# Kernel tuning notes

Hardware: AMD Instinct MI355X
Metric: run time of the kernel (lower is better)

## Reference

```python
import jax, jax.numpy as jnp
import numpy as np


def gcn_conv(x, edge_index, W, b):
    """PyG GCNConv: add self-loops, symmetric deg^{-1/2} normalization,
    linear transform, then scatter-add aggregation, plus bias."""
    n = x.shape[0]
    loops = jnp.arange(n, dtype=edge_index.dtype)
    src = jnp.concatenate([edge_index[0], loops])  # [E+N]
    dst = jnp.concatenate([edge_index[1], loops])
    ones = jnp.ones(src.shape[0], dtype=x.dtype)
    deg = jax.ops.segment_sum(ones, dst, num_segments=n)  # in-degree incl. self-loop
    dinv = jax.lax.rsqrt(jnp.maximum(deg, 1e-12))
    norm = dinv[src] * dinv[dst]  # [E+N]
    h = x @ W  # transform first (out_dim <= in_dim), [N, out]
    msg = h[src] * norm[:, None]  # gather + scale
    out = jax.ops.segment_sum(msg, dst, num_segments=n)  # scatter-add
    return out + b


def setup_inputs() -> dict:
    key = jax.random.key(0)
    ks = jax.random.split(key, 8)
    N, E, D_IN, D_OUT = 100000, 6400000, 32, 4
    x = jax.random.normal(ks[0], (N, D_IN), dtype=jnp.float32)
    edge_index = jax.random.randint(ks[1], (2, E), 0, N, dtype=jnp.int64)
    s1 = 1.0 / np.sqrt(D_IN)
    s2 = 1.0 / np.sqrt(16)
    s3 = 1.0 / np.sqrt(8)
    W1 = jax.random.uniform(ks[2], (D_IN, 16), jnp.float32, -s1, s1)
    b1 = jnp.zeros((16,), jnp.float32)
    W2 = jax.random.uniform(ks[3], (16, 8), jnp.float32, -s2, s2)
    b2 = jnp.zeros((8,), jnp.float32)
    Wfc = jax.random.uniform(ks[4], (8, D_OUT), jnp.float32, -s3, s3)
    bfc = jax.random.uniform(ks[5], (D_OUT,), jnp.float32, -s3, s3)
    return {"x": x, "edge_index": edge_index, "W1": W1, "b1": b1,
            "W2": W2, "b2": b2, "Wfc": Wfc, "bfc": bfc}


def reference(x, edge_index, W1, b1, W2, b2, Wfc, bfc):
    h = jax.nn.relu(gcn_conv(x, edge_index, W1, b1))
    h = jax.nn.relu(gcn_conv(h, edge_index, W2, b2))
    return h @ Wfc + bfc
```

## Files before the change

kernel.cpp:

```cpp
#include <hip/hip_runtime.h>
#include <hip/hip_fp16.h>

#define BLK 256
#define SHIFT 8
#define BSZ 256
#define MAXB 512
#define SRCBITS 17
#define SRCMASK ((1u << SRCBITS) - 1u)
#define TILE2 16384
#define BT 1024
#define LCAP 18432


__global__ __launch_bounds__(BT) void k_binA2(const int* __restrict__ src,
                                              const int* __restrict__ dst, int E, int N,
                                              unsigned* __restrict__ binned,
                                              int* __restrict__ bofs) {
    __shared__ int cnt[MAXB];
    __shared__ int sscan[MAXB];
    __shared__ int excl[MAXB];
    __shared__ unsigned sw[TILE2];
    int t = threadIdx.x;
    if (t < MAXB) cnt[t] = 0;
    __syncthreads();
    size_t tb = (size_t)blockIdx.x * TILE2;
    unsigned wv[16];
    int rkbk[16];
#pragma unroll
    for (int q = 0; q < 4; ++q) {
        int i4 = t + q * BT;
        size_t e0 = tb + (size_t)i4 * 4;
        int4 s4, d4;
        bool vec = (e0 + 4 <= (size_t)E);
        if (vec) {
            s4 = ((const int4*)src)[tb / 4 + i4];
            d4 = ((const int4*)dst)[tb / 4 + i4];
        }
#pragma unroll
        for (int j = 0; j < 4; ++j) {
            int idx = q * 4 + j;
            rkbk[idx] = -1;
            size_t e = e0 + j;
            int d = -1, s = -1;
            if (vec) {
                d = (j == 0) ? d4.x : (j == 1) ? d4.y : (j == 2) ? d4.z : d4.w;
                s = (j == 0) ? s4.x : (j == 1) ? s4.y : (j == 2) ? s4.z : s4.w;
            } else if (e < (size_t)E) {
                d = dst[e]; s = src[e];
            }
            if ((unsigned)d < (unsigned)N && (unsigned)s < (unsigned)N) {
                int b = d >> SHIFT;
                wv[idx] = (unsigned)s | ((unsigned)(d & (BSZ - 1)) << SRCBITS);
                int r = atomicAdd(&cnt[b], 1);
                rkbk[idx] = (r << 9) | b;
            }
        }
    }
    __syncthreads();
    if (t < MAXB) sscan[t] = cnt[t];
    __syncthreads();
    for (int off = 1; off < MAXB; off <<= 1) {
        int u = 0;
        if (t < MAXB && t >= off) u = sscan[t - off];
        __syncthreads();
        if (t < MAXB) sscan[t] += u;
        __syncthreads();
    }
    if (t < MAXB) excl[t] = sscan[t] - cnt[t];
    __syncthreads();
    int total = sscan[MAXB - 1];
#pragma unroll
    for (int idx = 0; idx < 16; ++idx) {
        int rb = rkbk[idx];
        if (rb >= 0) sw[excl[rb & 511] + (rb >> 9)] = wv[idx];
    }
    __syncthreads();
    int nq = total >> 2;
    for (int p = t; p < nq; p += BT) {
        uint4 v = *(const uint4*)&sw[p << 2];
        *(uint4*)(binned + tb + ((size_t)p << 2)) = v;
    }
    for (int p = (nq << 2) + t; p < total; p += BT) binned[tb + p] = sw[p];
    size_t bo = (size_t)blockIdx.x * (MAXB + 1);
    if (t < MAXB) bofs[bo + t] = excl[t];
    if (t == 0) bofs[bo + MAXB] = total;
}

__global__ __launch_bounds__(MAXB) void k_bsum(const int* __restrict__ bofs, int ntiles,
                                               int* __restrict__ btot) {
    int t = threadIdx.x;
    int c = 0;
    for (int tl = blockIdx.x; tl < ntiles; tl += gridDim.x) {
        size_t bo = (size_t)tl * (MAXB + 1);
        c += bofs[bo + t + 1] - bofs[bo + t];
    }
    if (c) atomicAdd(&btot[t], c);
}

__global__ __launch_bounds__(MAXB) void k_bscan(const int* __restrict__ btot,
                                                int* __restrict__ base) {
    __shared__ int s[MAXB];
    int t = threadIdx.x;
    int v = btot[t];
    s[t] = v;
    __syncthreads();
    for (int off = 1; off < MAXB; off <<= 1) {
        int u = (t >= off) ? s[t - off] : 0;
        __syncthreads();
        s[t] += u;
        __syncthreads();
    }
    base[t] = s[t] - v;
    if (t == MAXB - 1) base[MAXB] = s[t];
}


__global__ __launch_bounds__(1024) void k_buildB4(const unsigned* __restrict__ binned,
                                                  const int* __restrict__ bofs,
                                                  const int* __restrict__ baseB,
                                                  int ntiles, int N,
                                                  float* __restrict__ dinv,
                                                  int* __restrict__ rp,
                                                  unsigned* __restrict__ csr) {
    __shared__ int h[BSZ];
    __shared__ int sc[BSZ];
    __shared__ int cnt[BSZ];
    extern __shared__ unsigned lcsr[];
    int b = blockIdx.x;
    int t = threadIdx.x;
    int gb = b << SHIFT;
    if (t < BSZ) h[t] = 0;
    __syncthreads();
    int lane = t & 63, wid = t >> 6;
    int sub = lane >> 4, sl = lane & 15;
    for (int S = wid * 4 + sub; S < ntiles; S += 64) {
        size_t bo = (size_t)S * (MAXB + 1);
        int st = bofs[bo + b], en = bofs[bo + b + 1];
        size_t base = (size_t)S * TILE2;
        int k = st + sl;
        for (; k + 16 < en; k += 32) {
            unsigned v0 = binned[base + k];
            unsigned v1 = binned[base + k + 16];
            atomicAdd(&h[v0 >> SRCBITS], 1);
            atomicAdd(&h[v1 >> SRCBITS], 1);
        }
        if (k < en) atomicAdd(&h[binned[base + k] >> SRCBITS], 1);
    }
    __syncthreads();
    if (t < BSZ) sc[t] = h[t];
    __syncthreads();
    for (int off = 1; off < BSZ; off <<= 1) {
        int u = 0;
        if (t < BSZ && t >= off) u = sc[t - off];
        __syncthreads();
        if (t < BSZ) sc[t] += u;
        __syncthreads();
    }
    int bb = baseB[b];
    int total = sc[BSZ - 1];
    if (t < BSZ) {
        int v = h[t];
        int excl = sc[t] - v;
        int gnode = gb + t;
        if (gnode < N) {
            rp[gnode] = bb + excl;
            dinv[gnode] = rsqrtf((float)v + 1.0f);
        }
        if (t == BSZ - 1) {
            int endn = gb + BSZ;
            if (endn > N) endn = N;
            rp[endn] = bb + total;
        }
        cnt[t] = excl;
    }
    __syncthreads();
    bool big = (total > LCAP);
    for (int S = wid * 4 + sub; S < ntiles; S += 64) {
        size_t bo = (size_t)S * (MAXB + 1);
        int st = bofs[bo + b], en = bofs[bo + b + 1];
        size_t base = (size_t)S * TILE2;
        int k = st + sl;
        for (; k + 16 < en; k += 32) {
            unsigned v0 = binned[base + k];
            unsigned v1 = binned[base + k + 16];
            int p0 = atomicAdd(&cnt[v0 >> SRCBITS], 1);
            int p1 = atomicAdd(&cnt[v1 >> SRCBITS], 1);
            unsigned w0 = (v0 & SRCMASK) << 5;
            unsigned w1 = (v1 & SRCMASK) << 5;
            if (!big) { lcsr[p0] = w0; lcsr[p1] = w1; }
            else      { csr[bb + p0] = w0; csr[bb + p1] = w1; }
        }
        if (k < en) {
            unsigned v = binned[base + k];
            int pos = atomicAdd(&cnt[v >> SRCBITS], 1);
            unsigned w = (v & SRCMASK) << 5;
            if (!big) lcsr[pos] = w;
            else      csr[bb + pos] = w;
        }
    }
    __syncthreads();
    if (!big) {
        int h0 = ((bb + 3) & ~3) - bb;
        if (h0 > total) h0 = total;
        if (t < h0) csr[bb + t] = lcsr[t];
        int rem = total - h0;
        int nq = (rem > 0) ? (rem >> 2) : 0;
        for (int p = t; p < nq; p += 1024) {
            int lp = h0 + (p << 2);
            uint4 v = make_uint4(lcsr[lp], lcsr[lp + 1], lcsr[lp + 2], lcsr[lp + 3]);
            *(uint4*)(csr + bb + lp) = v;
        }
        for (int p = h0 + (nq << 2) + t; p < total; p += 1024) csr[bb + p] = lcsr[p];
    }
}


union Pk8 { __half h[8]; uint4 u; };
union H2U { unsigned u; __half2 h; };

__global__ __launch_bounds__(BLK) void k_transform1h(const float* __restrict__ x,
                                                     const float* __restrict__ W1,
                                                     const float* __restrict__ dinv,
                                                     __half* __restrict__ g1h, int N) {
    __shared__ float sW[32 * 16];
    for (int t = threadIdx.x; t < 512; t += BLK) sW[t] = W1[t];
    __syncthreads();
    int i = blockIdx.x * BLK + threadIdx.x;
    if (i >= N) return;
    float xr[32];
    const float4* xp = (const float4*)(x + (size_t)i * 32);
#pragma unroll
    for (int q = 0; q < 8; ++q) {
        float4 v = xp[q];
        xr[4*q] = v.x; xr[4*q+1] = v.y; xr[4*q+2] = v.z; xr[4*q+3] = v.w;
    }
    float di = dinv[i];
    Pk8 p0, p1;
#pragma unroll
    for (int j = 0; j < 16; ++j) {
        float a = 0.f;
#pragma unroll
        for (int k = 0; k < 32; ++k) a += xr[k] * sW[k * 16 + j];
        if (j < 8) p0.h[j] = __float2half_rn(a * di);
        else       p1.h[j - 8] = __float2half_rn(a * di);
    }
    uint4* gp = (uint4*)(g1h + (size_t)i * 16);
    gp[0] = p0.u;
    gp[1] = p1.u;
}


__global__ __launch_bounds__(BLK) void k_agg1(const int* __restrict__ rp,
                                              const unsigned* __restrict__ csr,
                                              const __half* __restrict__ g1h,
                                              const float* __restrict__ dinv,
                                              const float* __restrict__ b1,
                                              const float* __restrict__ W2,
                                              float* __restrict__ g2, int N) {
    __shared__ float sW[16 * 8];
    __shared__ float sb[16];
    if (threadIdx.x < 128) sW[threadIdx.x] = W2[threadIdx.x];
    if (threadIdx.x < 16) sb[threadIdx.x] = b1[threadIdx.x];
    __syncthreads();
    int wid = blockIdx.x * (BLK / 32) + (threadIdx.x >> 5);
    if (wid >= N) return;
    int alane = threadIdx.x & 63;
    int lane = threadIdx.x & 31;
    int c4 = lane & 3;
    int slot = lane >> 2;
    const char* gbase = (const char*)g1h;
    int foff = c4 << 3;
    int base_ = rp[wid], end = rp[wid + 1];
    float a0 = 0.f, a1 = 0.f, a2 = 0.f, a3 = 0.f;
    int k = base_ + slot;
    for (; k + 8 < end; k += 16) {
        unsigned v0 = csr[k], v1 = csr[k + 8];
        uint2 u0 = *(const uint2*)(gbase + v0 + foff);
        uint2 u1 = *(const uint2*)(gbase + v1 + foff);
        H2U x0, x1, y0, y1;
        x0.u = u0.x; y0.u = u0.y; x1.u = u1.x; y1.u = u1.y;
        float2 f0 = __half22float2(x0.h), f1 = __half22float2(y0.h);
        float2 f2 = __half22float2(x1.h), f3 = __half22float2(y1.h);
        a0 += f0.x + f2.x; a1 += f0.y + f2.y;
        a2 += f1.x + f3.x; a3 += f1.y + f3.y;
    }
    if (k < end) {
        unsigned v0 = csr[k];
        uint2 u0 = *(const uint2*)(gbase + v0 + foff);
        H2U x0, y0;
        x0.u = u0.x; y0.u = u0.y;
        float2 f0 = __half22float2(x0.h), f1 = __half22float2(y0.h);
        a0 += f0.x; a1 += f0.y; a2 += f1.x; a3 += f1.y;
    }
#pragma unroll
    for (int m = 4; m <= 16; m <<= 1) {
        a0 += __shfl_xor(a0, m);
        a1 += __shfl_xor(a1, m);
        a2 += __shfl_xor(a2, m);
        a3 += __shfl_xor(a3, m);
    }
    float di = dinv[wid];
    uint2 su = *(const uint2*)(gbase + ((size_t)wid << 5) + foff);
    H2U sx, sy;
    sx.u = su.x; sy.u = su.y;
    float2 sf0 = __half22float2(sx.h), sf1 = __half22float2(sy.h);
    float hh[4];
    hh[0] = fmaxf((a0 + sf0.x) * di + sb[4*c4+0], 0.f);
    hh[1] = fmaxf((a1 + sf0.y) * di + sb[4*c4+1], 0.f);
    hh[2] = fmaxf((a2 + sf1.x) * di + sb[4*c4+2], 0.f);
    hh[3] = fmaxf((a3 + sf1.y) * di + sb[4*c4+3], 0.f);
    int g4 = alane & ~3;
    int o = lane & 7;
    float a = 0.f;
#pragma unroll
    for (int kk = 0; kk < 16; ++kk) {
        float hv = __shfl(hh[kk & 3], g4 + (kk >> 2));
        a += hv * sW[kk * 8 + o];
    }
    if (lane < 8) g2[(size_t)wid * 8 + lane] = a * di;
}

__global__ __launch_bounds__(BLK) void k_agg2(const int* __restrict__ rp,
                                              const unsigned* __restrict__ csr,
                                              const float* __restrict__ g2,
                                              const float* __restrict__ dinv,
                                              const float* __restrict__ b2,
                                              const float* __restrict__ Wfc,
                                              const float* __restrict__ bfc,
                                              float* __restrict__ out, int N) {
    __shared__ float sW[8 * 4];
    __shared__ float sb2[8];
    __shared__ float sbf[4];
    if (threadIdx.x < 32) sW[threadIdx.x] = Wfc[threadIdx.x];
    if (threadIdx.x < 8) sb2[threadIdx.x] = b2[threadIdx.x];
    if (threadIdx.x < 4) sbf[threadIdx.x] = bfc[threadIdx.x];
    __syncthreads();
    int wid = blockIdx.x * (BLK / 32) + (threadIdx.x >> 5);
    if (wid >= N) return;
    int alane = threadIdx.x & 63;
    int lane = threadIdx.x & 31;
    int c4 = lane & 3;
    int slot = lane >> 2;
    const char* gbase = (const char*)g2;
    int foff = c4 << 3;
    int base_ = rp[wid], end = rp[wid + 1];
    float a0 = 0.f, a1 = 0.f;
    int k = base_ + slot;
    for (; k + 8 < end; k += 16) {
        unsigned v0 = csr[k], v1 = csr[k + 8];
        float2 f0 = *(const float2*)(gbase + v0 + foff);
        float2 f1 = *(const float2*)(gbase + v1 + foff);
        a0 += f0.x + f1.x;
        a1 += f0.y + f1.y;
    }
    if (k < end) {
        unsigned v0 = csr[k];
        float2 f0 = *(const float2*)(gbase + v0 + foff);
        a0 += f0.x; a1 += f0.y;
    }
#pragma unroll
    for (int m = 4; m <= 16; m <<= 1) {
        a0 += __shfl_xor(a0, m);
        a1 += __shfl_xor(a1, m);
    }
    float di = dinv[wid];
    float2 sf = *(const float2*)(gbase + ((size_t)wid << 5) + foff);
    float hh[2];
    hh[0] = fmaxf((a0 + sf.x) * di + sb2[2*c4+0], 0.f);
    hh[1] = fmaxf((a1 + sf.y) * di + sb2[2*c4+1], 0.f);
    int g4 = alane & ~3;
    int o = lane & 3;
    float a = 0.f;
#pragma unroll
    for (int j = 0; j < 8; ++j) {
        float hv = __shfl(hh[j & 1], g4 + (j >> 1));
        a += hv * sW[j * 4 + o];
    }
    if (lane < 4) out[(size_t)wid * 4 + lane] = a + sbf[lane];
}


__global__ __launch_bounds__(BLK) void k_count(const int* __restrict__ dst, int E, int N,
                                               float* __restrict__ cnt) {
    int i = blockIdx.x * BLK + threadIdx.x;
    if (i < E) {
        int d = dst[i];
        if ((unsigned)d < (unsigned)N) atomicAdd(&cnt[d], 1.0f);
    }
}
__global__ __launch_bounds__(BLK) void k_dinv_f(float* __restrict__ cnt, int N) {
    int i = blockIdx.x * BLK + threadIdx.x;
    if (i < N) cnt[i] = rsqrtf(cnt[i] + 1.0f);
}
__global__ __launch_bounds__(BLK) void k_transform1(const float* __restrict__ x,
                                                    const float* __restrict__ W1,
                                                    const float* __restrict__ dinv,
                                                    float* __restrict__ g1, int N) {
    __shared__ float sW[32 * 16];
    for (int t = threadIdx.x; t < 512; t += BLK) sW[t] = W1[t];
    __syncthreads();
    int i = blockIdx.x * BLK + threadIdx.x;
    if (i >= N) return;
    float xr[32];
    const float4* xp = (const float4*)(x + (size_t)i * 32);
#pragma unroll
    for (int q = 0; q < 8; ++q) {
        float4 v = xp[q];
        xr[4*q] = v.x; xr[4*q+1] = v.y; xr[4*q+2] = v.z; xr[4*q+3] = v.w;
    }
    float di = dinv[i];
    float o[16];
#pragma unroll
    for (int j = 0; j < 16; ++j) {
        float a = 0.f;
#pragma unroll
        for (int k = 0; k < 32; ++k) a += xr[k] * sW[k * 16 + j];
        o[j] = a * di;
    }
    float4* gp = (float4*)(g1 + (size_t)i * 16);
#pragma unroll
    for (int q = 0; q < 4; ++q)
        gp[q] = make_float4(o[4*q], o[4*q+1], o[4*q+2], o[4*q+3]);
}
template <int F>
__global__ __launch_bounds__(BLK) void k_edge_agg(const int* __restrict__ src,
                                                  const int* __restrict__ dst,
                                                  int E, int N,
                                                  const float* __restrict__ g,
                                                  float* __restrict__ agg) {
    size_t t = (size_t)blockIdx.x * BLK + threadIdx.x;
    int e = (int)(t / F);
    int f = (int)(t & (F - 1));
    if (e >= E) return;
    int s = src[e], d = dst[e];
    if ((unsigned)s >= (unsigned)N || (unsigned)d >= (unsigned)N) return;
    atomicAdd(&agg[(size_t)d * F + f], g[(size_t)s * F + f]);
}
__global__ __launch_bounds__(BLK) void k_node1(const float* __restrict__ g1,
                                               const float* __restrict__ agg1,
                                               const float* __restrict__ dinv,
                                               const float* __restrict__ b1,
                                               const float* __restrict__ W2,
                                               float* __restrict__ g2, int N) {
    __shared__ float sW[16 * 8];
    __shared__ float sb[16];
    for (int t = threadIdx.x; t < 128; t += BLK) sW[t] = W2[t];
    if (threadIdx.x < 16) sb[threadIdx.x] = b1[threadIdx.x];
    __syncthreads();
    int i = blockIdx.x * BLK + threadIdx.x;
    if (i >= N) return;
    float di = dinv[i];
    const float4* gp = (const float4*)(g1 + (size_t)i * 16);
    const float4* ap = (const float4*)(agg1 + (size_t)i * 16);
    float h[16];
#pragma unroll
    for (int q = 0; q < 4; ++q) {
        float4 gv = gp[q], av = ap[q];
        h[4*q+0] = fmaxf((av.x + gv.x) * di + sb[4*q+0], 0.f);
        h[4*q+1] = fmaxf((av.y + gv.y) * di + sb[4*q+1], 0.f);
        h[4*q+2] = fmaxf((av.z + gv.z) * di + sb[4*q+2], 0.f);
        h[4*q+3] = fmaxf((av.w + gv.w) * di + sb[4*q+3], 0.f);
    }
    float o[8];
#pragma unroll
    for (int j = 0; j < 8; ++j) {
        float a = 0.f;
#pragma unroll
        for (int k = 0; k < 16; ++k) a += h[k] * sW[k * 8 + j];
        o[j] = a * di;
    }
    float4* op = (float4*)(g2 + (size_t)i * 8);
    op[0] = make_float4(o[0], o[1], o[2], o[3]);
    op[1] = make_float4(o[4], o[5], o[6], o[7]);
}
__global__ __launch_bounds__(BLK) void k_node2(const float* __restrict__ g2,
                                               const float* __restrict__ agg2,
                                               const float* __restrict__ dinv,
                                               const float* __restrict__ b2,
                                               const float* __restrict__ Wfc,
                                               const float* __restrict__ bfc,
                                               float* __restrict__ out, int N) {
    __shared__ float sW[8 * 4];
    __shared__ float sb2[8];
    __shared__ float sbf[4];
    if (threadIdx.x < 32) sW[threadIdx.x] = Wfc[threadIdx.x];
    if (threadIdx.x < 8) sb2[threadIdx.x] = b2[threadIdx.x];
    if (threadIdx.x < 4) sbf[threadIdx.x] = bfc[threadIdx.x];
    __syncthreads();
    int i = blockIdx.x * BLK + threadIdx.x;
    if (i >= N) return;
    float di = dinv[i];
    const float4* gp = (const float4*)(g2 + (size_t)i * 8);
    const float4* ap = (const float4*)(agg2 + (size_t)i * 8);
    float h[8];
#pragma unroll
    for (int q = 0; q < 2; ++q) {
        float4 gv = gp[q], av = ap[q];
        h[4*q+0] = fmaxf((av.x + gv.x) * di + sb2[4*q+0], 0.f);
        h[4*q+1] = fmaxf((av.y + gv.y) * di + sb2[4*q+1], 0.f);
        h[4*q+2] = fmaxf((av.z + gv.z) * di + sb2[4*q+2], 0.f);
        h[4*q+3] = fmaxf((av.w + gv.w) * di + sb2[4*q+3], 0.f);
    }
    float o[4];
#pragma unroll
    for (int k = 0; k < 4; ++k) {
        float a = sbf[k];
#pragma unroll
        for (int j = 0; j < 8; ++j) a += h[j] * sW[j * 4 + k];
        o[k] = a;
    }
    ((float4*)(out + (size_t)i * 4))[0] = make_float4(o[0], o[1], o[2], o[3]);
}


extern "C" void kernel_launch(void* const* d_in, const int* in_sizes, int n_in,
                              void* d_out, int out_size, void* d_ws, size_t ws_size,
                              hipStream_t stream) {
    const float* x   = (const float*)d_in[0];
    const int*   ei  = (const int*)d_in[1];
    const float* W1  = (const float*)d_in[2];
    const float* b1  = (const float*)d_in[3];
    const float* W2  = (const float*)d_in[4];
    const float* b2  = (const float*)d_in[5];
    const float* Wfc = (const float*)d_in[6];
    const float* bfc = (const float*)d_in[7];

    int N = in_sizes[0] / 32;
    int E = in_sizes[1] / 2;
    const int* src = ei;
    const int* dst = ei + (size_t)E;

    int ntiles = (E + TILE2 - 1) / TILE2;
    int nbuk = (N + BSZ - 1) >> SHIFT;

    size_t w_g1h  = 0;
    size_t w_g2   = w_g1h + (size_t)8 * N;
    size_t w_dinv = w_g2 + (size_t)8 * N;
    size_t w_rp   = w_dinv + (size_t)N;
    size_t w_btot = w_rp + (size_t)N + 1;
    size_t w_bs   = w_btot + MAXB;
    size_t w_bofs = w_bs + MAXB + 1;
    size_t w_bin  = (w_bofs + (size_t)ntiles * (MAXB + 1) + 3) & ~(size_t)3;
    size_t w_csr  = (w_bin + (size_t)E + 3) & ~(size_t)3;
    size_t need   = (w_csr + (size_t)E + 4) * 4;

    bool fast = (ws_size >= need) && (N <= (1 << SRCBITS)) && (nbuk <= MAXB);

    if (fast) {
        float*    ws     = (float*)d_ws;
        __half*   g1h    = (__half*)(ws + w_g1h);
        float*    g2     = ws + w_g2;
        float*    dinv   = ws + w_dinv;
        int*      rp     = (int*)(ws + w_rp);
        int*      btot   = (int*)(ws + w_btot);
        int*      baseB  = (int*)(ws + w_bs);
        int*      bofs   = (int*)(ws + w_bofs);
        unsigned* binned = (unsigned*)(ws + w_bin);
        unsigned* csr    = (unsigned*)(ws + w_csr);

        int nnode = (N + BLK - 1) / BLK;
        int nagg = (N + (BLK / 32) - 1) / (BLK / 32);

        hipMemsetAsync(btot, 0, MAXB * 4, stream);

        k_binA2<<<ntiles, BT, 0, stream>>>(src, dst, E, N, binned, bofs);
        k_bsum<<<128, MAXB, 0, stream>>>(bofs, ntiles, btot);
        k_bscan<<<1, MAXB, 0, stream>>>(btot, baseB);
        k_buildB4<<<nbuk, 1024, LCAP * 4, stream>>>(binned, bofs, baseB,
                                                    ntiles, N, dinv, rp, csr);
        k_transform1h<<<nnode, BLK, 0, stream>>>(x, W1, dinv, g1h, N);
        k_agg1<<<nagg, BLK, 0, stream>>>(rp, csr, g1h, dinv, b1, W2, g2, N);
        k_agg2<<<nagg, BLK, 0, stream>>>(rp, csr, g2, dinv, b2, Wfc, bfc,
                                         (float*)d_out, N);
    } else {
        float* ws   = (float*)d_ws;
        float* dinv = ws;
        float* g1   = dinv + (size_t)N;
        float* agg1 = g1 + (size_t)16 * N;
        float* g2   = agg1 + (size_t)16 * N;
        float* agg2 = g2 + (size_t)8 * N;

        hipMemsetAsync(dinv, 0, (size_t)N * 4, stream);
        hipMemsetAsync(agg1, 0, (size_t)16 * N * 4, stream);
        hipMemsetAsync(agg2, 0, (size_t)8 * N * 4, stream);

        k_count<<<(E + BLK - 1) / BLK, BLK, 0, stream>>>(dst, E, N, dinv);
        k_dinv_f<<<(N + BLK - 1) / BLK, BLK, 0, stream>>>(dinv, N);
        k_transform1<<<(N + BLK - 1) / BLK, BLK, 0, stream>>>(x, W1, dinv, g1, N);
        {
            size_t tot = (size_t)E * 16;
            k_edge_agg<16><<<(unsigned)((tot + BLK - 1) / BLK), BLK, 0, stream>>>(src, dst, E, N, g1, agg1);
        }
        k_node1<<<(N + BLK - 1) / BLK, BLK, 0, stream>>>(g1, agg1, dinv, b1, W2, g2, N);
        {
            size_t tot = (size_t)E * 8;
            k_edge_agg<8><<<(unsigned)((tot + BLK - 1) / BLK), BLK, 0, stream>>>(src, dst, E, N, g2, agg2);
        }
        k_node2<<<(N + BLK - 1) / BLK, BLK, 0, stream>>>(g2, agg2, dinv, b2, Wfc, bfc, (float*)d_out, N);
    }
}
```

Baseline: 160.7 us.

## Stage binned edges in LDS during histogram pass to avoid second global read

The CSR build kernel now copies each bucket's binned edges into a linear LDS buffer during the histogram pass. It first runs a per-block prefix scan over tile segment lengths so each tile's segment lands at a known offset in that buffer. The scatter pass then reads from LDS instead of re-reading the binned array from global memory. In exchange, the LDS footprint roughly doubles, which likely allows only one block per CU and may spread the 391 buckets over two waves. The extra scan and the loss of 2-way unrolling also add overhead.

```diff
diff --git a/kernel.cpp b/kernel.cpp
--- a/kernel.cpp
+++ b/kernel.cpp
@@ -9,7 +9,7 @@
 #define SRCMASK ((1u << SRCBITS) - 1u)
 #define TILE2 16384
 #define BT 1024
-#define LCAP 18432
+#define LINCAP 18688
 
 
 __global__ __launch_bounds__(BT) void k_binA2(const int* __restrict__ src,
@@ -115,7 +115,7 @@
 }
 
 
-__global__ __launch_bounds__(1024) void k_buildB4(const unsigned* __restrict__ binned,
+__global__ __launch_bounds__(1024) void k_buildB5(const unsigned* __restrict__ binned,
                                                   const int* __restrict__ bofs,
                                                   const int* __restrict__ baseB,
                                                   int ntiles, int N,
@@ -125,26 +125,50 @@
     __shared__ int h[BSZ];
     __shared__ int sc[BSZ];
     __shared__ int cnt[BSZ];
-    extern __shared__ unsigned lcsr[];
+    __shared__ int segstart[1024];
+    extern __shared__ unsigned dyn[];
+    unsigned* lin  = dyn;
+    unsigned* lcsr = dyn + LINCAP;
     int b = blockIdx.x;
     int t = threadIdx.x;
     int gb = b << SHIFT;
+    int len = 0;
+    if (t < ntiles) {
+        size_t bo = (size_t)t * (MAXB + 1);
+        len = bofs[bo + b + 1] - bofs[bo + b];
+    }
+    segstart[t] = len;
+    __syncthreads();
+    for (int off = 1; off < 1024; off <<= 1) {
+        int u = (t >= off) ? segstart[t - off] : 0;
+        __syncthreads();
+        segstart[t] += u;
+        __syncthreads();
+    }
+    int total = segstart[1023];
+    int myexcl = segstart[t] - len;
+    __syncthreads();
+    segstart[t] = myexcl;
     if (t < BSZ) h[t] = 0;
     __syncthreads();
+    bool big = (total > LINCAP);
     int lane = t & 63, wid = t >> 6;
     int sub = lane >> 4, sl = lane & 15;
     for (int S = wid * 4 + sub; S < ntiles; S += 64) {
         size_t bo = (size_t)S * (MAXB + 1);
         int st = bofs[bo + b], en = bofs[bo + b + 1];
         size_t base = (size_t)S * TILE2;
-        int k = st + sl;
-        for (; k + 16 < en; k += 32) {
-            unsigned v0 = binned[base + k];
-            unsigned v1 = binned[base + k + 16];
-            atomicAdd(&h[v0 >> SRCBITS], 1);
-            atomicAdd(&h[v1 >> SRCBITS], 1);
-        }
-        if (k < en) atomicAdd(&h[binned[base + k] >> SRCBITS], 1);
+        int ls = segstart[S];
+        if (!big) {
+            for (int k = st + sl; k < en; k += 16) {
+                unsigned v = binned[base + k];
+                lin[ls + (k - st)] = v;
+                atomicAdd(&h[v >> SRCBITS], 1);
+            }
+        } else {
+            for (int k = st + sl; k < en; k += 16)
+                atomicAdd(&h[binned[base + k] >> SRCBITS], 1);
+        }
     }
     __syncthreads();
     if (t < BSZ) sc[t] = h[t];
@@ -157,7 +181,6 @@
         __syncthreads();
     }
     int bb = baseB[b];
-    int total = sc[BSZ - 1];
     if (t < BSZ) {
         int v = h[t];
         int excl = sc[t] - v;
@@ -174,32 +197,13 @@
         cnt[t] = excl;
     }
     __syncthreads();
-    bool big = (total > LCAP);
-    for (int S = wid * 4 + sub; S < ntiles; S += 64) {
-        size_t bo = (size_t)S * (MAXB + 1);
-        int st = bofs[bo + b], en = bofs[bo + b + 1];
-        size_t base = (size_t)S * TILE2;
-        int k = st + sl;
-        for (; k + 16 < en; k += 32) {
-            unsigned v0 = binned[base + k];
-            unsigned v1 = binned[base + k + 16];
-            int p0 = atomicAdd(&cnt[v0 >> SRCBITS], 1);
-            int p1 = atomicAdd(&cnt[v1 >> SRCBITS], 1);
-            unsigned w0 = (v0 & SRCMASK) << 5;
-            unsigned w1 = (v1 & SRCMASK) << 5;
-            if (!big) { lcsr[p0] = w0; lcsr[p1] = w1; }
-            else      { csr[bb + p0] = w0; csr[bb + p1] = w1; }
-        }
-        if (k < en) {
-            unsigned v = binned[base + k];
+    if (!big) {
+        for (int p = t; p < total; p += 1024) {
+            unsigned v = lin[p];
             int pos = atomicAdd(&cnt[v >> SRCBITS], 1);
-            unsigned w = (v & SRCMASK) << 5;
-            if (!big) lcsr[pos] = w;
-            else      csr[bb + pos] = w;
-        }
-    }
-    __syncthreads();
-    if (!big) {
+            lcsr[pos] = (v & SRCMASK) << 5;
+        }
+        __syncthreads();
         int h0 = ((bb + 3) & ~3) - bb;
         if (h0 > total) h0 = total;
         if (t < h0) csr[bb + t] = lcsr[t];
@@ -211,6 +215,17 @@
             *(uint4*)(csr + bb + lp) = v;
         }
         for (int p = h0 + (nq << 2) + t; p < total; p += 1024) csr[bb + p] = lcsr[p];
+    } else {
+        for (int S = wid * 4 + sub; S < ntiles; S += 64) {
+            size_t bo = (size_t)S * (MAXB + 1);
+            int st = bofs[bo + b], en = bofs[bo + b + 1];
+            size_t base = (size_t)S * TILE2;
+            for (int k = st + sl; k < en; k += 16) {
+                unsigned v = binned[base + k];
+                int pos = atomicAdd(&cnt[v >> SRCBITS], 1);
+                csr[bb + pos] = (v & SRCMASK) << 5;
+            }
+        }
     }
 }
 
@@ -544,7 +559,8 @@
     size_t w_csr  = (w_bin + (size_t)E + 3) & ~(size_t)3;
     size_t need   = (w_csr + (size_t)E + 4) * 4;
 
-    bool fast = (ws_size >= need) && (N <= (1 << SRCBITS)) && (nbuk <= MAXB);
+    bool fast = (ws_size >= need) && (N <= (1 << SRCBITS)) && (nbuk <= MAXB)
+                && (ntiles <= 1024);
 
     if (fast) {
         float*    ws     = (float*)d_ws;
@@ -566,8 +582,8 @@
         k_binA2<<<ntiles, BT, 0, stream>>>(src, dst, E, N, binned, bofs);
         k_bsum<<<128, MAXB, 0, stream>>>(bofs, ntiles, btot);
         k_bscan<<<1, MAXB, 0, stream>>>(btot, baseB);
-        k_buildB4<<<nbuk, 1024, LCAP * 4, stream>>>(binned, bofs, baseB,
-                                                    ntiles, N, dinv, rp, csr);
+        k_buildB5<<<nbuk, 1024, 2 * LINCAP * 4, stream>>>(binned, bofs, baseB,
+                                                          ntiles, N, dinv, rp, csr);
         k_transform1h<<<nnode, BLK, 0, stream>>>(x, W1, dinv, g1h, N);
         k_agg1<<<nagg, BLK, 0, stream>>>(rp, csr, g1h, dinv, b1, W2, g2, N);
         k_agg2<<<nagg, BLK, 0, stream>>>(rp, csr, g2, dinv, b2, Wfc, bfc,
```

Result: slower. 169.2 us (+5.3%).
